# Optimization experiments

Hardware: AMD Instinct MI355X
Metric: run time of the kernel (lower is better)

## Reference

```python
import jax, jax.numpy as jnp
import numpy as np

N_NODES = 100000
E_HALF = 1600000
N_EDGES = 2 * E_HALF
D = 32        # node feature dim
OUT = 32      # out_features


def setup_inputs() -> dict:
    key = jax.random.key(0)
    ks = jax.random.split(key, 8)
    h = jax.random.normal(ks[0], (N_NODES, D), dtype=jnp.float32)
    couplings = jax.random.normal(ks[1], (E_HALF,), dtype=jnp.float32)
    senders = jax.random.randint(ks[2], (N_EDGES,), 0, N_NODES)
    receivers = jax.random.randint(ks[3], (N_EDGES,), 0, N_NODES)
    # Dense params (LeCun-normal-ish init)
    W1 = jax.random.normal(ks[4], (2 * D + 1, OUT), dtype=jnp.float32) / jnp.sqrt(2.0 * D + 1.0)
    b1 = jnp.zeros((OUT,), dtype=jnp.float32)
    Wq = jax.random.normal(ks[5], (D, OUT), dtype=jnp.float32) / jnp.sqrt(1.0 * D)
    bq = jnp.zeros((OUT,), dtype=jnp.float32)
    Wk = jax.random.normal(ks[6], (D, OUT), dtype=jnp.float32) / jnp.sqrt(1.0 * D)
    bk = jnp.zeros((OUT,), dtype=jnp.float32)
    return {"h": h, "couplings": couplings, "W1": W1, "b1": b1,
            "Wq": Wq, "bq": bq, "Wk": Wk, "bk": bk,
            "senders": senders, "receivers": receivers}


def reference(h, couplings, W1, b1, Wq, bq, Wk, bk, senders, receivers):
    # gather endpoint features: [E, D]
    rf = h[receivers, :]
    sf = h[senders, :]
    # couplings duplicated (one copy per edge direction): [E, 1]
    mc = jnp.concatenate([couplings, couplings])[:, None]
    edge_features = jnp.concatenate([rf, sf, mc], axis=-1)   # [E, 2D+1]
    messages = jax.nn.relu(edge_features @ W1 + b1)          # [E, OUT]
    # attention gate: sigmoid(<q, k>)
    q = sf @ Wq + bq
    k = rf @ Wk + bk
    a = jnp.sum(q * k, axis=-1, keepdims=True)               # [E, 1]
    messages = messages * jax.nn.sigmoid(a)
    aggregated = jax.ops.segment_sum(messages, receivers, num_segments=h.shape[0])  # [N, OUT]
    return jax.nn.relu(aggregated)
```

## Files before the change

kernel.cpp:

```cpp
#include <hip/hip_runtime.h>
#include <hip/hip_bf16.h>
#include <cstdint>


#define EPG 8

__device__ __forceinline__ float bf16lo(uint32_t u) {
    uint32_t b = (u & 0xFFFFu) << 16;
    float f; __builtin_memcpy(&f, &b, 4); return f;
}
__device__ __forceinline__ float bf16hi(uint32_t u) {
    uint32_t b = u & 0xFFFF0000u;
    float f; __builtin_memcpy(&f, &b, 4); return f;
}
__device__ __forceinline__ uint32_t pack_bf16(float lo, float hi) {
    __hip_bfloat16 l = __float2bfloat16(lo);
    __hip_bfloat16 h = __float2bfloat16(hi);
    uint16_t lb, hb;
    __builtin_memcpy(&lb, &l, 2);
    __builtin_memcpy(&hb, &h, 2);
    return (uint32_t)lb | ((uint32_t)hb << 16);
}

__device__ __forceinline__ void atomic_pk_add_bf16(uint32_t* addr, uint32_t val) {
    asm volatile("global_atomic_pk_add_bf16 %0, %1, off" :: "v"(addr), "v"(val) : "memory");
}


__global__ __launch_bounds__(256) void node_precompute(
    const float* __restrict__ h, const float* __restrict__ W1,
    const float* __restrict__ b1, const float* __restrict__ Wq,
    const float* __restrict__ bq, const float* __restrict__ Wk,
    const float* __restrict__ bk,
    uint32_t* __restrict__ Ak, uint32_t* __restrict__ Bq, int n_nodes)
{
    __shared__ float sW[4][32 * 33];
    int tid = threadIdx.x;
    for (int i = tid; i < 1024; i += 256) {
        int j = i >> 5, t = i & 31;
        sW[0][j * 33 + t] = W1[i];
        sW[1][j * 33 + t] = W1[1024 + i];
        sW[2][j * 33 + t] = Wq[i];
        sW[3][j * 33 + t] = Wk[i];
    }
    __syncthreads();

    int t    = tid & 31;
    int wave = tid >> 6;
    int half = wave & 1;
    int sub  = (tid >> 5) & 1;
    int nib  = (wave >> 1) * 2 + sub;

    int ma = half ? 1 : 0;
    int mb = half ? 2 : 3;
    float wa[32], wb[32];
    #pragma unroll
    for (int j = 0; j < 32; ++j) {
        wa[j] = sW[ma][j * 33 + t];
        wb[j] = sW[mb][j * 33 + t];
    }
    float ba = half ? 0.f    : b1[t];
    float bb = half ? bq[t]  : bk[t];
    uint32_t* dst = half ? Bq : Ak;

    for (int n = blockIdx.x * 4 + nib; n < n_nodes; n += gridDim.x * 4) {
        float hv = h[n * 32 + t];
        float aa = ba, ab = bb;
        #pragma unroll
        for (int j = 0; j < 32; ++j) {
            float hj = __shfl(hv, j, 32);
            aa = fmaf(hj, wa[j], aa);
            ab = fmaf(hj, wb[j], ab);
        }
        dst[n * 32 + t] = pack_bf16(aa, ab);
    }
}


__global__ __launch_bounds__(256) void edge_kernel(
    const uint32_t* __restrict__ Ak, const uint32_t* __restrict__ Bq,
    const int* __restrict__ senders, const int* __restrict__ receivers,
    const float* __restrict__ couplings, const float* __restrict__ W1,
    uint32_t* __restrict__ agg, int n_edges, int e_half)
{
    int lane = threadIdx.x & 15;
    int sg   = (blockIdx.x * 256 + threadIdx.x) >> 4;
    float w0 = W1[64 * 32 + 2 * lane];
    float w1 = W1[64 * 32 + 2 * lane + 1];
    int e0 = sg * EPG;
    if (e0 >= n_edges) return;

    int r[EPG], s[EPG];
    float c[EPG];

    if (e0 + EPG <= n_edges) {
        int4 ra = *(const int4*)(receivers + e0);
        int4 rb = *(const int4*)(receivers + e0 + 4);
        int4 sa = *(const int4*)(senders + e0);
        int4 sb = *(const int4*)(senders + e0 + 4);
        int cb = (e0 < e_half) ? e0 : e0 - e_half;
        float4 ca  = *(const float4*)(couplings + cb);
        float4 cb4 = *(const float4*)(couplings + cb + 4);
        r[0]=ra.x; r[1]=ra.y; r[2]=ra.z; r[3]=ra.w;
        r[4]=rb.x; r[5]=rb.y; r[6]=rb.z; r[7]=rb.w;
        s[0]=sa.x; s[1]=sa.y; s[2]=sa.z; s[3]=sa.w;
        s[4]=sb.x; s[5]=sb.y; s[6]=sb.z; s[7]=sb.w;
        c[0]=ca.x; c[1]=ca.y; c[2]=ca.z; c[3]=ca.w;
        c[4]=cb4.x; c[5]=cb4.y; c[6]=cb4.z; c[7]=cb4.w;
    } else {
        #pragma unroll
        for (int j = 0; j < EPG; ++j) {
            int e = e0 + j;
            if (e < n_edges) {
                r[j] = receivers[e];
                s[j] = senders[e];
                c[j] = couplings[e < e_half ? e : e - e_half];
            } else { r[j] = 0; s[j] = 0; c[j] = 0.f; }
        }
    }

    uint2 ak[EPG], bq[EPG];
    #pragma unroll
    for (int j = 0; j < EPG; ++j) ak[j] = ((const uint2*)Ak)[(size_t)r[j] * 16 + lane];
    #pragma unroll
    for (int j = 0; j < EPG; ++j) bq[j] = ((const uint2*)Bq)[(size_t)s[j] * 16 + lane];

    #pragma unroll
    for (int j = 0; j < EPG; ++j) {
        float A0 = bf16lo(ak[j].x), k0 = bf16hi(ak[j].x);
        float A1 = bf16lo(ak[j].y), k1 = bf16hi(ak[j].y);
        float B0 = bf16lo(bq[j].x), q0 = bf16hi(bq[j].x);
        float B1 = bf16lo(bq[j].y), q1 = bf16hi(bq[j].y);

        float m0 = fmaxf(fmaf(c[j], w0, A0 + B0), 0.f);
        float m1 = fmaxf(fmaf(c[j], w1, A1 + B1), 0.f);

        float d = fmaf(q0, k0, q1 * k1);
        d += __shfl_xor(d, 1, 64);
        d += __shfl_xor(d, 2, 64);
        d += __shfl_xor(d, 4, 64);
        d += __shfl_xor(d, 8, 64);

        if (d > -8.f && e0 + j < n_edges) {
            float sig = __fdividef(1.f, 1.f + __expf(-d));
            uint32_t val = pack_bf16(m0 * sig, m1 * sig);
            atomic_pk_add_bf16(agg + (size_t)r[j] * 16 + lane, val);
        }
    }
}

__global__ __launch_bounds__(256) void relu_widen_copy(
    const uint2* __restrict__ agg, float4* __restrict__ out, int n4)
{
    int i = blockIdx.x * 256 + threadIdx.x;
    if (i < n4) {
        uint2 v = agg[i];
        float4 o;
        o.x = fmaxf(bf16lo(v.x), 0.f);
        o.y = fmaxf(bf16hi(v.x), 0.f);
        o.z = fmaxf(bf16lo(v.y), 0.f);
        o.w = fmaxf(bf16hi(v.y), 0.f);
        out[i] = o;
    }
}

extern "C" void kernel_launch(void* const* d_in, const int* in_sizes, int n_in,
                              void* d_out, int out_size, void* d_ws, size_t ws_size,
                              hipStream_t stream)
{
    const float* h         = (const float*)d_in[0];
    const float* couplings = (const float*)d_in[1];
    const float* W1        = (const float*)d_in[2];
    const float* b1        = (const float*)d_in[3];
    const float* Wq        = (const float*)d_in[4];
    const float* bq        = (const float*)d_in[5];
    const float* Wk        = (const float*)d_in[6];
    const float* bk        = (const float*)d_in[7];
    const int*   senders   = (const int*)d_in[8];
    const int*   receivers = (const int*)d_in[9];
    float* out = (float*)d_out;

    int n_nodes = in_sizes[0] / 32;
    int e_half  = in_sizes[1];
    int n_edges = in_sizes[8];

    size_t N32 = (size_t)n_nodes * 32;

    uint32_t* Ak  = (uint32_t*)d_ws;
    uint32_t* Bq  = Ak + N32;
    uint32_t* agg = Bq + N32;

    hipMemsetAsync(agg, 0, N32 * 2, stream);

    node_precompute<<<2048, 256, 0, stream>>>(
        h, W1, b1, Wq, bq, Wk, bk, Ak, Bq, n_nodes);

    int nsub    = (n_edges + EPG - 1) / EPG;
    int eblocks = (nsub + 15) / 16;
    edge_kernel<<<eblocks, 256, 0, stream>>>(
        Ak, Bq, senders, receivers, couplings, W1, agg, n_edges, e_half);

    int n4 = (int)(N32 / 4);
    relu_widen_copy<<<(n4 + 255) / 256, 256, 0, stream>>>(
        (const uint2*)agg, (float4*)out, n4);
}
```

Baseline: 291.3 us.

## Fold agg zeroing into precompute, double edges per group, use nontemporal index loads

Removes the separate memset launch by zeroing the bf16 aggregation buffer inside the node precompute kernel. Doubles edges per 16-lane subgroup to 16 so more independent gathers are in flight, and loads sender, receiver and coupling indices with nontemporal hints to avoid polluting cache. Adds a straddle check so a group that crosses the e_half boundary falls back to scalar coupling loads. The larger group raises register use, which may lower occupancy.

```diff
diff --git a/kernel.cpp b/kernel.cpp
--- a/kernel.cpp
+++ b/kernel.cpp
@@ -3,7 +3,10 @@
 #include <cstdint>
 
 
-#define EPG 8
+#define EPG 16
+
+typedef int   vint4   __attribute__((ext_vector_type(4)));
+typedef float vfloat4 __attribute__((ext_vector_type(4)));
 
 __device__ __forceinline__ float bf16lo(uint32_t u) {
     uint32_t b = (u & 0xFFFFu) << 16;
@@ -32,8 +35,12 @@
     const float* __restrict__ b1, const float* __restrict__ Wq,
     const float* __restrict__ bq, const float* __restrict__ Wk,
     const float* __restrict__ bk,
-    uint32_t* __restrict__ Ak, uint32_t* __restrict__ Bq, int n_nodes)
-{
+    uint32_t* __restrict__ Ak, uint32_t* __restrict__ Bq,
+    uint4* __restrict__ aggz, int n_aggz, int n_nodes)
+{
+    for (int i = blockIdx.x * 256 + threadIdx.x; i < n_aggz; i += gridDim.x * 256)
+        aggz[i] = make_uint4(0u, 0u, 0u, 0u);
+
     __shared__ float sW[4][32 * 33];
     int tid = threadIdx.x;
     for (int i = tid; i < 1024; i += 256) {
@@ -93,20 +100,21 @@
     int r[EPG], s[EPG];
     float c[EPG];
 
-    if (e0 + EPG <= n_edges) {
-        int4 ra = *(const int4*)(receivers + e0);
-        int4 rb = *(const int4*)(receivers + e0 + 4);
-        int4 sa = *(const int4*)(senders + e0);
-        int4 sb = *(const int4*)(senders + e0 + 4);
+    bool straddle = (e0 < e_half) && (e0 + EPG > e_half);
+    if (e0 + EPG <= n_edges && !straddle) {
+        #pragma unroll
+        for (int v = 0; v < EPG / 4; ++v) {
+            vint4 rv = __builtin_nontemporal_load((const vint4*)(receivers + e0) + v);
+            vint4 sv = __builtin_nontemporal_load((const vint4*)(senders   + e0) + v);
+            r[4*v+0]=rv.x; r[4*v+1]=rv.y; r[4*v+2]=rv.z; r[4*v+3]=rv.w;
+            s[4*v+0]=sv.x; s[4*v+1]=sv.y; s[4*v+2]=sv.z; s[4*v+3]=sv.w;
+        }
         int cb = (e0 < e_half) ? e0 : e0 - e_half;
-        float4 ca  = *(const float4*)(couplings + cb);
-        float4 cb4 = *(const float4*)(couplings + cb + 4);
-        r[0]=ra.x; r[1]=ra.y; r[2]=ra.z; r[3]=ra.w;
-        r[4]=rb.x; r[5]=rb.y; r[6]=rb.z; r[7]=rb.w;
-        s[0]=sa.x; s[1]=sa.y; s[2]=sa.z; s[3]=sa.w;
-        s[4]=sb.x; s[5]=sb.y; s[6]=sb.z; s[7]=sb.w;
-        c[0]=ca.x; c[1]=ca.y; c[2]=ca.z; c[3]=ca.w;
-        c[4]=cb4.x; c[5]=cb4.y; c[6]=cb4.z; c[7]=cb4.w;
+        #pragma unroll
+        for (int v = 0; v < EPG / 4; ++v) {
+            vfloat4 cv = __builtin_nontemporal_load((const vfloat4*)(couplings + cb) + v);
+            c[4*v+0]=cv.x; c[4*v+1]=cv.y; c[4*v+2]=cv.z; c[4*v+3]=cv.w;
+        }
     } else {
         #pragma unroll
         for (int j = 0; j < EPG; ++j) {
@@ -189,11 +197,10 @@
     uint32_t* Ak  = (uint32_t*)d_ws;
     uint32_t* Bq  = Ak + N32;
     uint32_t* agg = Bq + N32;
-
-    hipMemsetAsync(agg, 0, N32 * 2, stream);
+    int n_aggz = (int)(N32 / 8);
 
     node_precompute<<<2048, 256, 0, stream>>>(
-        h, W1, b1, Wq, bq, Wk, bk, Ak, Bq, n_nodes);
+        h, W1, b1, Wq, bq, Wk, bk, Ak, Bq, (uint4*)agg, n_aggz, n_nodes);
 
     int nsub    = (n_edges + EPG - 1) / EPG;
     int eblocks = (nsub + 15) / 16;
```

Result: no change. 295.6 us (+1.5%).
